# Optimization experiments

Hardware: AMD Instinct MI355X
Metric: run time of the kernel (lower is better)

Reference implementation:

```python
import jax, jax.numpy as jnp
import numpy as np

NHOP = 3

def setup_inputs() -> dict:
    key = jax.random.key(0)
    kq, kk, kv, kw, kb = jax.random.split(key, 5)
    B, Lq, Lk, D = 16, 512, 2048, 1024
    Q = jax.random.normal(kq, (B, Lq, D), dtype=jnp.float32)
    K = jax.random.normal(kk, (B, Lk, D), dtype=jnp.float32)
    V = jax.random.normal(kv, (B, Lk, D), dtype=jnp.float32)
    # nn.Linear(2D, D): weight [D, 2D], bias [D]
    W = jax.random.normal(kw, (D, 2 * D), dtype=jnp.float32) * (1.0 / np.sqrt(2 * D))
    b = jax.random.normal(kb, (D,), dtype=jnp.float32) * 0.01
    return {"Q": Q, "K": K, "V": V, "W": W, "b": b}


def reference(Q, K, V, W, b):
    D = Q.shape[-1]
    scale = 1.0 / jnp.sqrt(jnp.asarray(D, dtype=Q.dtype))
    Q_hop = Q
    attn = None
    for _ in range(NHOP):
        # [B, Lq, Lk]
        scores = jnp.einsum("bqd,bkd->bqk", Q_hop, K) * scale
        attn = jax.nn.softmax(scores, axis=-1)
        R = jnp.einsum("bqk,bkd->bqd", attn, V)          # [B, Lq, D]
        cat = jnp.concatenate([Q_hop, R], axis=-1)       # [B, Lq, 2D]
        Q_hop = jnp.tanh(jnp.einsum("bqe,de->bqd", cat, W) + b)
    return (Q_hop, attn)
```

## Files before the change

kernel.cpp:

```cpp
#include <hip/hip_runtime.h>
#include <math.h>

#define NB 16
#define LQ 512
#define LKK 2048
#define DD 1024

typedef _Float16 half8 __attribute__((ext_vector_type(8)));
typedef _Float16 half4 __attribute__((ext_vector_type(4)));
typedef float f32x4 __attribute__((ext_vector_type(4)));

__device__ __forceinline__ void gl_lds16(const void* g, void* l) {
    __builtin_amdgcn_global_load_lds(
        (const __attribute__((address_space(1))) void*)g,
        (__attribute__((address_space(3))) void*)l, 16, 0, 0);
}

__global__ __launch_bounds__(512, 2) void gemm_qk_256(
    const _Float16* __restrict__ A, long sA,
    const _Float16* __restrict__ B, long sB,
    _Float16* __restrict__ P, long sP,
    float* __restrict__ partial,
    float scale)
{
    __shared__ _Float16 lsA[2][256 * 64];
    __shared__ _Float16 lsB[2][256 * 64];
    const int tid = threadIdx.x;
    const int w = tid >> 6, l = tid & 63;
    const int wr = w >> 2, wc = w & 3;
    const int lrg = l >> 4, lc = l & 15, lr = lrg << 2;

    int id = blockIdx.x + gridDim.x * (blockIdx.y + gridDim.y * blockIdx.z);
    const int nwg = gridDim.x * gridDim.y * gridDim.z;
    id = (id & 7) * (nwg >> 3) + (id >> 3);
    const int bx = id % gridDim.x;
    const int t2 = id / gridDim.x;
    const int by = t2 % gridDim.y;
    const int z  = t2 / gridDim.y;
    const int m0 = by * 256, n0 = bx * 256;

    const _Float16* Ab = A + (size_t)z * sA + (size_t)m0 * DD;
    const _Float16* Bb = B + (size_t)z * sB + (size_t)n0 * DD;

    const int srow = l >> 3;
    const int sk = ((l & 7) ^ srow) << 3;

#define STG(dst, srcbase)                                                     \
    do {                                                                      \
        _Pragma("unroll")                                                     \
        for (int rr = 0; rr < 2; ++rr) {                                      \
            const int c = w + 8 * rr;                                         \
            gl_lds16((srcbase) + (size_t)(c * 8 + srow) * DD + sk,            \
                     (dst) + c * 512);                                        \
        }                                                                     \
    } while (0)

    half8 af[4][2], bf01[2][2], bf23[2][2];
    f32x4 acc[8][4] = {};
    const int rsb = (lc & 7) << 4;

#define LDA(buf, mh)                                                          \
    do {                                                                      \
        const char* p_ = (const char*)lsA[buf];                               \
        _Pragma("unroll")                                                     \
        for (int ii = 0; ii < 4; ++ii) {                                      \
            const int row_ = wr * 128 + (mh) * 64 + ii * 16 + lc;             \
            _Pragma("unroll")                                                 \
            for (int kk = 0; kk < 2; ++kk)                                    \
                af[ii][kk] = *(const half8*)(p_ + row_ * 128 +                \
                             ((kk * 64 + (lrg << 4)) ^ rsb));                 \
        }                                                                     \
    } while (0)

#define LDB(buf, nh, bfr)                                                     \
    do {                                                                      \
        const char* p_ = (const char*)lsB[buf];                               \
        _Pragma("unroll")                                                     \
        for (int jj = 0; jj < 2; ++jj) {                                      \
            const int row_ = wc * 64 + ((nh) * 2 + jj) * 16 + lc;             \
            _Pragma("unroll")                                                 \
            for (int kk = 0; kk < 2; ++kk)                                    \
                bfr[jj][kk] = *(const half8*)(p_ + row_ * 128 +               \
                              ((kk * 64 + (lrg << 4)) ^ rsb));                \
        }                                                                     \
    } while (0)

#define MM(mh, nh, bfr)                                                       \
    do {                                                                      \
        __builtin_amdgcn_s_setprio(1);                                        \
        _Pragma("unroll")                                                     \
        for (int ii = 0; ii < 4; ++ii)                                        \
            _Pragma("unroll")                                                 \
            for (int jj = 0; jj < 2; ++jj)                                    \
                _Pragma("unroll")                                             \
                for (int kk = 0; kk < 2; ++kk)                                \
                    acc[(mh) * 4 + ii][(nh) * 2 + jj] =                       \
                        __builtin_amdgcn_mfma_f32_16x16x32_f16(               \
                            af[ii][kk], bfr[jj][kk],                          \
                            acc[(mh) * 4 + ii][(nh) * 2 + jj], 0, 0, 0);      \
        __builtin_amdgcn_s_setprio(0);                                        \
    } while (0)

#define BAR __builtin_amdgcn_s_barrier()
#define VMW(n) asm volatile("s_waitcnt vmcnt(" #n ")" ::: "memory")

    STG(&lsA[0][0], Ab);
    STG(&lsA[0][128 * 64], Ab + (size_t)128 * DD);
    STG(&lsB[0][0], Bb);
    STG(&lsB[0][128 * 64], Bb + (size_t)128 * DD);
    STG(&lsA[1][0], Ab + 64);
    VMW(2);
    BAR;

    for (int i = 0; i < 7; ++i) {
        const int kt1 = (2 * i + 1) * 64, kt2 = kt1 + 64, kt3 = kt2 + 64;
        LDA(0, 0); LDB(0, 0, bf01);
        STG(&lsA[1][128 * 64], Ab + (size_t)128 * DD + kt1);
        BAR; MM(0, 0, bf01); BAR;
        LDB(0, 1, bf23);
        STG(&lsB[1][0], Bb + kt1);
        BAR; MM(0, 1, bf23); BAR;
        LDA(0, 1);
        STG(&lsB[1][128 * 64], Bb + (size_t)128 * DD + kt1);
        BAR; MM(1, 0, bf01); BAR;
        STG(&lsA[0][0], Ab + kt2);
        BAR; MM(1, 1, bf23);
        VMW(2); BAR;
        LDA(1, 0); LDB(1, 0, bf01);
        STG(&lsA[0][128 * 64], Ab + (size_t)128 * DD + kt2);
        BAR; MM(0, 0, bf01); BAR;
        LDB(1, 1, bf23);
        STG(&lsB[0][0], Bb + kt2);
        BAR; MM(0, 1, bf23); BAR;
        LDA(1, 1);
        STG(&lsB[0][128 * 64], Bb + (size_t)128 * DD + kt2);
        BAR; MM(1, 0, bf01); BAR;
        STG(&lsA[1][0], Ab + kt3);
        BAR; MM(1, 1, bf23);
        VMW(2); BAR;
    }
    {
        const int kt1 = 15 * 64;
        LDA(0, 0); LDB(0, 0, bf01);
        STG(&lsA[1][128 * 64], Ab + (size_t)128 * DD + kt1);
        BAR; MM(0, 0, bf01); BAR;
        LDB(0, 1, bf23);
        STG(&lsB[1][0], Bb + kt1);
        BAR; MM(0, 1, bf23); BAR;
        LDA(0, 1);
        STG(&lsB[1][128 * 64], Bb + (size_t)128 * DD + kt1);
        BAR; MM(1, 0, bf01); BAR;
        BAR; MM(1, 1, bf23);
        VMW(0); BAR;
        LDA(1, 0); LDB(1, 0, bf01);
        BAR; MM(0, 0, bf01); BAR;
        LDB(1, 1, bf23);
        BAR; MM(0, 1, bf23); BAR;
        LDA(1, 1);
        BAR; MM(1, 0, bf01); BAR;
        BAR; MM(1, 1, bf23);
    }
    __syncthreads();

    _Float16* Cb = P + (size_t)z * sP;
    float* psum = (float*)&lsA[0][0];
    #pragma unroll
    for (int i = 0; i < 8; ++i) {
        float rsum[4] = {0.f, 0.f, 0.f, 0.f};
        #pragma unroll
        for (int j = 0; j < 4; ++j) {
            const int n = n0 + wc * 64 + j * 16 + lc;
            #pragma unroll
            for (int r = 0; r < 4; ++r) {
                const int m = m0 + wr * 128 + i * 16 + lr + r;
                const float e = __expf(acc[i][j][r] * scale);
                Cb[(size_t)m * LKK + n] = (_Float16)e;
                rsum[r] += e;
            }
        }
        #pragma unroll
        for (int r = 0; r < 4; ++r) {
            float s = rsum[r];
            s += __shfl_xor(s, 1);
            s += __shfl_xor(s, 2);
            s += __shfl_xor(s, 4);
            s += __shfl_xor(s, 8);
            if (lc == 0) psum[(wr * 128 + i * 16 + lr + r) * 4 + wc] = s;
        }
    }
    __syncthreads();
    if (tid < 256) {
        const float* pr = psum + tid * 4;
        partial[((size_t)z * LQ + m0 + tid) * 8 + bx] = pr[0] + pr[1] + pr[2] + pr[3];
    }
#undef STG
#undef LDA
#undef LDB
#undef MM
}

__global__ __launch_bounds__(512, 2) void gemm_pc_256x128(
    const _Float16* __restrict__ Alo, long sAlo, int lda_lo,
    const _Float16* __restrict__ Ahi, long sAhi, int lda_hi,
    int ksplit,
    const _Float16* __restrict__ B, long sB, int ldb,
    int K, int mode,
    float* __restrict__ out32, long s32, int ldc32,
    _Float16* __restrict__ out16, long s16, int ldc16,
    const float* __restrict__ bias,
    const float* __restrict__ partial, int npart)
{
    __shared__ _Float16 ls[3][384 * 64];
    const int tid = threadIdx.x;
    const int w = tid >> 6, l = tid & 63;
    const int wr = w >> 2, wc = w & 3;
    const int lrg = l >> 4, lc = l & 15, lr = lrg << 2;

    int id = blockIdx.x + gridDim.x * (blockIdx.y + gridDim.y * blockIdx.z);
    const int nwg = gridDim.x * gridDim.y * gridDim.z;
    id = (id & 7) * (nwg >> 3) + (id >> 3);
    const int bx = id % gridDim.x;
    const int t2_ = id / gridDim.x;
    const int by = t2_ % gridDim.y;
    const int z  = t2_ / gridDim.y;
    const int m0 = by * 256, n0 = bx * 128;

    const _Float16* Abase_lo = Alo + (size_t)z * sAlo + (size_t)m0 * lda_lo;
    const _Float16* Abase_hi = Ahi ? (Ahi + (size_t)z * sAhi + (size_t)m0 * lda_hi) : (const _Float16*)0;
    const _Float16* Bbase = B + (size_t)z * sB + (size_t)n0 * ldb;

    const int srow = l >> 3;
    const int sk = ((l & 7) ^ srow) << 3;
    const int rsb = (lc & 7) << 4;

    half8 af[4][2], bf[2][2];
    f32x4 acc[8][2] = {};

#define STGA(tt, dbuf)                                                        \
    do {                                                                      \
        const int kb_ = (tt) * 64;                                            \
        const _Float16* s_; int ld_;                                          \
        if (kb_ < ksplit) { s_ = Abase_lo + kb_;           ld_ = lda_lo; }    \
        else              { s_ = Abase_hi + (kb_ - ksplit); ld_ = lda_hi; }   \
        _Float16* d_ = &ls[dbuf][0];                                          \
        _Pragma("unroll")                                                     \
        for (int rr = 0; rr < 4; ++rr) {                                      \
            const int c = w + 8 * rr;                                         \
            gl_lds16(s_ + (size_t)(c * 8 + srow) * ld_ + sk, d_ + c * 512);   \
        }                                                                     \
    } while (0)

#define STGB(tt, dbuf)                                                        \
    do {                                                                      \
        const _Float16* s_ = Bbase + (tt) * 64;                               \
        _Float16* d_ = &ls[dbuf][256 * 64];                                   \
        _Pragma("unroll")                                                     \
        for (int rr = 0; rr < 2; ++rr) {                                      \
            const int c = w + 8 * rr;                                         \
            gl_lds16(s_ + (size_t)(c * 8 + srow) * ldb + sk, d_ + c * 512);   \
        }                                                                     \
    } while (0)

#define LDA2(buf, mh)                                                         \
    do {                                                                      \
        const char* p_ = (const char*)&ls[buf][0];                            \
        _Pragma("unroll")                                                     \
        for (int ii = 0; ii < 4; ++ii) {                                      \
            const int row_ = wr * 128 + (mh) * 64 + ii * 16 + lc;             \
            _Pragma("unroll")                                                 \
            for (int kk = 0; kk < 2; ++kk)                                    \
                af[ii][kk] = *(const half8*)(p_ + row_ * 128 +                \
                             ((kk * 64 + (lrg << 4)) ^ rsb));                 \
        }                                                                     \
    } while (0)

#define LDB2(buf)                                                             \
    do {                                                                      \
        const char* p_ = (const char*)&ls[buf][256 * 64];                     \
        _Pragma("unroll")                                                     \
        for (int jj = 0; jj < 2; ++jj) {                                      \
            const int row_ = wc * 32 + jj * 16 + lc;                          \
            _Pragma("unroll")                                                 \
            for (int kk = 0; kk < 2; ++kk)                                    \
                bf[jj][kk] = *(const half8*)(p_ + row_ * 128 +                \
                              ((kk * 64 + (lrg << 4)) ^ rsb));                \
        }                                                                     \
    } while (0)

#define MM2(mh)                                                               \
    do {                                                                      \
        __builtin_amdgcn_s_setprio(1);                                        \
        _Pragma("unroll")                                                     \
        for (int ii = 0; ii < 4; ++ii)                                        \
            _Pragma("unroll")                                                 \
            for (int jj = 0; jj < 2; ++jj)                                    \
                _Pragma("unroll")                                             \
                for (int kk = 0; kk < 2; ++kk)                                \
                    acc[(mh) * 4 + ii][jj] =                                  \
                        __builtin_amdgcn_mfma_f32_16x16x32_f16(               \
                            af[ii][kk], bf[jj][kk],                           \
                            acc[(mh) * 4 + ii][jj], 0, 0, 0);                 \
        __builtin_amdgcn_s_setprio(0);                                        \
    } while (0)

    const int NT = K >> 6;
    STGA(0, 0); STGB(0, 0);
    STGA(1, 1); STGB(1, 1);
    VMW(6);
    BAR;

    int b = 0, b2 = 2;
    for (int t = 0; t < NT; ++t) {
        const int tt = t + 2;
        const bool st = tt < NT;
        LDA2(b, 0); LDB2(b);
        if (st) STGA(tt, b2);
        BAR; MM2(0); BAR;
        LDA2(b, 1);
        if (st) STGB(tt, b2);
        BAR; MM2(1);
        if (t < NT - 2)       VMW(6);
        else if (t == NT - 2) VMW(0);
        BAR;
        b = (b == 2) ? 0 : b + 1;
        b2 = (b2 == 2) ? 0 : b2 + 1;
    }
    __syncthreads();

    if (mode == 1) {
        float* psum = (float*)&ls[0][0];
        if (tid < 256) {
            const float* pp = partial + ((size_t)z * LQ + m0 + tid) * npart;
            float s = 0.0f;
            for (int c = 0; c < npart; ++c) s += pp[c];
            psum[tid] = 1.0f / s;
        }
        __syncthreads();
        _Float16* Cb = out16 + (size_t)z * s16;
        #pragma unroll
        for (int i = 0; i < 8; ++i)
            #pragma unroll
            for (int j = 0; j < 2; ++j) {
                const int n = n0 + wc * 32 + j * 16 + lc;
                #pragma unroll
                for (int r = 0; r < 4; ++r) {
                    const int ml = wr * 128 + i * 16 + lr + r;
                    Cb[(size_t)(m0 + ml) * ldc16 + n] =
                        (_Float16)(acc[i][j][r] * psum[ml]);
                }
            }
    } else {
        float bv[2];
        #pragma unroll
        for (int j = 0; j < 2; ++j)
            bv[j] = bias[n0 + wc * 32 + j * 16 + lc];
        #pragma unroll
        for (int i = 0; i < 8; ++i)
            #pragma unroll
            for (int j = 0; j < 2; ++j) {
                const int n = n0 + wc * 32 + j * 16 + lc;
                #pragma unroll
                for (int r = 0; r < 4; ++r) {
                    const int m = m0 + wr * 128 + i * 16 + lr + r;
                    const float t = tanhf(acc[i][j][r] + bv[j]);
                    if (out16) out16[(size_t)z * s16 + (size_t)m * ldc16 + n] = (_Float16)t;
                    if (out32) out32[(size_t)z * s32 + (size_t)m * ldc32 + n] = t;
                }
            }
    }
#undef STGA
#undef STGB
#undef LDA2
#undef LDB2
#undef MM2
#undef BAR
#undef VMW
}

__global__ __launch_bounds__(256) void gemm_f16_nt(
    const _Float16* __restrict__ Alo, long sAlo, int lda_lo,
    const _Float16* __restrict__ Ahi, long sAhi, int lda_hi,
    int ksplit,
    const _Float16* __restrict__ B, long sB, int ldb,
    int K, int mode, float scale,
    float* __restrict__ out32, long s32, int ldc32,
    _Float16* __restrict__ out16, long s16, int ldc16,
    const float* __restrict__ bias,
    float* __restrict__ partial, const float* __restrict__ inv, int npart)
{
    __shared__ _Float16 lsA[128 * 64];
    __shared__ _Float16 lsB[128 * 64];
    __shared__ float psum[128][2];
    const int tid = threadIdx.x;
    const int w = tid >> 6, l = tid & 63;
    const int wr = w >> 1, wc = w & 1;

    int id = blockIdx.x + gridDim.x * (blockIdx.y + gridDim.y * blockIdx.z);
    const int nwg = gridDim.x * gridDim.y * gridDim.z;
    id = (id & 7) * (nwg >> 3) + (id >> 3);
    const int bx = id % gridDim.x;
    const int t2 = id / gridDim.x;
    const int by = t2 % gridDim.y;
    const int z = t2 / gridDim.y;
    const int m0 = by * 128, n0 = bx * 128;

    const _Float16* Abase_lo = Alo + (size_t)z * sAlo + (size_t)m0 * lda_lo;
    const _Float16* Abase_hi = Ahi ? (Ahi + (size_t)z * sAhi + (size_t)m0 * lda_hi) : (const _Float16*)0;
    const _Float16* Bbase = B + (size_t)z * sB + (size_t)n0 * ldb;

    const int srow = l >> 3;
    const int sswz = ((l & 7) ^ srow) << 3;

    f32x4 acc[4][4] = {};

    for (int k0 = 0; k0 < K; k0 += 64) {
        const _Float16* Ap; int kloc, ldaA;
        if (k0 < ksplit) { Ap = Abase_lo; kloc = k0;          ldaA = lda_lo; }
        else             { Ap = Abase_hi; kloc = k0 - ksplit; ldaA = lda_hi; }
        #pragma unroll
        for (int i = 0; i < 4; ++i) {
            const int c = w * 4 + i;
            const int row = c * 8 + srow;
            gl_lds16(Ap + (size_t)row * ldaA + kloc + sswz, &lsA[c * 512]);
        }
        #pragma unroll
        for (int i = 0; i < 4; ++i) {
            const int c = w * 4 + i;
            const int row = c * 8 + srow;
            gl_lds16(Bbase + (size_t)row * ldb + k0 + sswz, &lsB[c * 512]);
        }
        __syncthreads();

        half8 af[4][2], bf[4][2];
        const char* lA = (const char*)lsA;
        const char* lB = (const char*)lsB;
        const int rs = (l & 7) << 4;
        const int cb = (l >> 4) << 4;
        #pragma unroll
        for (int i = 0; i < 4; ++i) {
            const int rowa = wr * 64 + i * 16 + (l & 15);
            const int rowb = wc * 64 + i * 16 + (l & 15);
            #pragma unroll
            for (int kk = 0; kk < 2; ++kk) {
                af[i][kk] = *(const half8*)(lA + rowa * 128 + ((kk * 64 + cb) ^ rs));
                bf[i][kk] = *(const half8*)(lB + rowb * 128 + ((kk * 64 + cb) ^ rs));
            }
        }
        #pragma unroll
        for (int kk = 0; kk < 2; ++kk)
            #pragma unroll
            for (int i = 0; i < 4; ++i)
                #pragma unroll
                for (int j = 0; j < 4; ++j)
                    acc[i][j] = __builtin_amdgcn_mfma_f32_16x16x32_f16(
                        af[i][kk], bf[j][kk], acc[i][j], 0, 0, 0);
        __syncthreads();
    }

    const int lr = (l >> 4) * 4;
    const int lc = l & 15;
    if (mode == 0) {
        _Float16* Cb = out16 + (size_t)z * s16;
        float rsum[4][4];
        #pragma unroll
        for (int i = 0; i < 4; ++i)
            #pragma unroll
            for (int r = 0; r < 4; ++r) rsum[i][r] = 0.0f;
        #pragma unroll
        for (int i = 0; i < 4; ++i)
            #pragma unroll
            for (int j = 0; j < 4; ++j) {
                const int n = n0 + wc * 64 + j * 16 + lc;
                #pragma unroll
                for (int r = 0; r < 4; ++r) {
                    const int m = m0 + wr * 64 + i * 16 + lr + r;
                    const float e = __expf(acc[i][j][r] * scale);
                    Cb[(size_t)m * ldc16 + n] = (_Float16)e;
                    rsum[i][r] += e;
                }
            }
        #pragma unroll
        for (int i = 0; i < 4; ++i)
            #pragma unroll
            for (int r = 0; r < 4; ++r) {
                float s = rsum[i][r];
                s += __shfl_xor(s, 1);
                s += __shfl_xor(s, 2);
                s += __shfl_xor(s, 4);
                s += __shfl_xor(s, 8);
                rsum[i][r] = s;
            }
        if (lc == 0) {
            #pragma unroll
            for (int i = 0; i < 4; ++i)
                #pragma unroll
                for (int r = 0; r < 4; ++r)
                    psum[wr * 64 + i * 16 + lr + r][wc] = rsum[i][r];
        }
        __syncthreads();
        if (tid < 128)
            partial[((size_t)z * LQ + m0 + tid) * npart + bx] = psum[tid][0] + psum[tid][1];
    } else if (mode == 1) {
        _Float16* Cb = out16 + (size_t)z * s16;
        float iv[4][4];
        if (partial) {
            if (tid < 128) {
                const float* pp = partial + ((size_t)z * LQ + m0 + tid) * npart;
                float s = 0.0f;
                for (int c = 0; c < npart; ++c) s += pp[c];
                psum[tid][0] = 1.0f / s;
            }
            __syncthreads();
            #pragma unroll
            for (int i = 0; i < 4; ++i)
                #pragma unroll
                for (int r = 0; r < 4; ++r)
                    iv[i][r] = psum[wr * 64 + i * 16 + lr + r][0];
        } else {
            #pragma unroll
            for (int i = 0; i < 4; ++i)
                #pragma unroll
                for (int r = 0; r < 4; ++r)
                    iv[i][r] = inv ? inv[(size_t)z * LQ + m0 + wr * 64 + i * 16 + lr + r] : 1.0f;
        }
        #pragma unroll
        for (int i = 0; i < 4; ++i)
            #pragma unroll
            for (int j = 0; j < 4; ++j) {
                const int n = n0 + wc * 64 + j * 16 + lc;
                #pragma unroll
                for (int r = 0; r < 4; ++r) {
                    const int m = m0 + wr * 64 + i * 16 + lr + r;
                    Cb[(size_t)m * ldc16 + n] = (_Float16)(acc[i][j][r] * iv[i][r]);
                }
            }
    } else if (mode == 4) {
        float* Cb = out32 + (size_t)z * s32;
        #pragma unroll
        for (int i = 0; i < 4; ++i)
            #pragma unroll
            for (int j = 0; j < 4; ++j) {
                const int n = n0 + wc * 64 + j * 16 + lc;
                #pragma unroll
                for (int r = 0; r < 4; ++r) {
                    const int m = m0 + wr * 64 + i * 16 + lr + r;
                    Cb[(size_t)m * ldc32 + n] = acc[i][j][r] * scale;
                }
            }
    } else {
        float bv[4];
        #pragma unroll
        for (int j = 0; j < 4; ++j)
            bv[j] = bias[n0 + wc * 64 + j * 16 + lc];
        #pragma unroll
        for (int i = 0; i < 4; ++i)
            #pragma unroll
            for (int j = 0; j < 4; ++j) {
                const int n = n0 + wc * 64 + j * 16 + lc;
                #pragma unroll
                for (int r = 0; r < 4; ++r) {
                    const int m = m0 + wr * 64 + i * 16 + lr + r;
                    const float t = tanhf(acc[i][j][r] + bv[j]);
                    if (out16) out16[(size_t)z * s16 + (size_t)m * ldc16 + n] = (_Float16)t;
                    if (out32) out32[(size_t)z * s32 + (size_t)m * ldc32 + n] = t;
                }
            }
    }
}

__global__ __launch_bounds__(256) void scale_attn(
    const _Float16* __restrict__ P, const float* __restrict__ partial,
    float* __restrict__ attn, int npart)
{
    __shared__ float sinv;
    const long row = blockIdx.x;
    const int tid = threadIdx.x;
    if (tid < npart) {
        float s = partial[row * npart + tid];
        for (int off = npart >> 1; off > 0; off >>= 1) s += __shfl_xor(s, off);
        if (tid == 0) sinv = 1.0f / s;
    }
    __syncthreads();
    const float inv = sinv;
    const half8 h = *(const half8*)(P + row * 2048 + tid * 8);
    float* o = attn + row * 2048 + tid * 8;
    float4 a = make_float4((float)h[0] * inv, (float)h[1] * inv,
                           (float)h[2] * inv, (float)h[3] * inv);
    float4 b = make_float4((float)h[4] * inv, (float)h[5] * inv,
                           (float)h[6] * inv, (float)h[7] * inv);
    *(float4*)o = a;
    *(float4*)(o + 4) = b;
}

__global__ __launch_bounds__(256) void make_inv(
    const float* __restrict__ partial, float* __restrict__ inv)
{
    const int row = blockIdx.x * 256 + threadIdx.x;
    const float4 a = *(const float4*)(partial + (size_t)row * 16);
    const float4 b = *(const float4*)(partial + (size_t)row * 16 + 4);
    const float4 c = *(const float4*)(partial + (size_t)row * 16 + 8);
    const float4 d = *(const float4*)(partial + (size_t)row * 16 + 12);
    const float s = (a.x + a.y + a.z + a.w) + (b.x + b.y + b.z + b.w)
                  + (c.x + c.y + c.z + c.w) + (d.x + d.y + d.z + d.w);
    inv[row] = 1.0f / s;
}

__global__ __launch_bounds__(256) void softmax_rows2(
    float* __restrict__ S, _Float16* __restrict__ f16out,
    long f16stride, int write_f32)
{
    __shared__ float red[8];
    const long row = blockIdx.x;
    float* p = S + row * LKK;
    const int tid = threadIdx.x;
    float4 v0 = ((const float4*)p)[tid];
    float4 v1 = ((const float4*)p)[tid + 256];
    float m = fmaxf(fmaxf(fmaxf(v0.x, v0.y), fmaxf(v0.z, v0.w)),
                    fmaxf(fmaxf(v1.x, v1.y), fmaxf(v1.z, v1.w)));
    #pragma unroll
    for (int off = 32; off > 0; off >>= 1) m = fmaxf(m, __shfl_down(m, off));
    if ((tid & 63) == 0) red[tid >> 6] = m;
    __syncthreads();
    m = fmaxf(fmaxf(red[0], red[1]), fmaxf(red[2], red[3]));
    v0.x = expf(v0.x - m); v0.y = expf(v0.y - m);
    v0.z = expf(v0.z - m); v0.w = expf(v0.w - m);
    v1.x = expf(v1.x - m); v1.y = expf(v1.y - m);
    v1.z = expf(v1.z - m); v1.w = expf(v1.w - m);
    float s = v0.x + v0.y + v0.z + v0.w + v1.x + v1.y + v1.z + v1.w;
    #pragma unroll
    for (int off = 32; off > 0; off >>= 1) s += __shfl_down(s, off);
    if ((tid & 63) == 0) red[4 + (tid >> 6)] = s;
    __syncthreads();
    s = red[4] + red[5] + red[6] + red[7];
    const float inv = 1.0f / s;
    v0.x *= inv; v0.y *= inv; v0.z *= inv; v0.w *= inv;
    v1.x *= inv; v1.y *= inv; v1.z *= inv; v1.w *= inv;
    if (write_f32) {
        ((float4*)p)[tid] = v0;
        ((float4*)p)[tid + 256] = v1;
    }
    _Float16* q = f16out + row * f16stride;
    half4 h0 = { (_Float16)v0.x, (_Float16)v0.y, (_Float16)v0.z, (_Float16)v0.w };
    half4 h1 = { (_Float16)v1.x, (_Float16)v1.y, (_Float16)v1.z, (_Float16)v1.w };
    *(half4*)(q + tid * 4) = h0;
    *(half4*)(q + 1024 + tid * 4) = h1;
}

__global__ __launch_bounds__(256) void cvt_f32_to_f16(
    const float* __restrict__ in, _Float16* __restrict__ out, long n)
{
    const long i = ((long)blockIdx.x * 256 + threadIdx.x) * 8;
    if (i + 8 > n) return;
    float4 a = *(const float4*)(in + i);
    float4 b = *(const float4*)(in + i + 4);
    half8 h = { (_Float16)a.x, (_Float16)a.y, (_Float16)a.z, (_Float16)a.w,
                (_Float16)b.x, (_Float16)b.y, (_Float16)b.z, (_Float16)b.w };
    *(half8*)(out + i) = h;
}

__global__ __launch_bounds__(256) void transpose_cvt_v(
    const float* __restrict__ V, _Float16* __restrict__ Vt)
{
    __shared__ _Float16 t[64][80];
    const int z = blockIdx.z;
    const int k0 = blockIdx.y * 64, d0 = blockIdx.x * 64;
    const float* Vb = V + (size_t)z * LKK * DD;
    _Float16* Vtb = Vt + (size_t)z * DD * LKK;
    const int r = threadIdx.x >> 2;
    const int c0 = (threadIdx.x & 3) * 16;
    #pragma unroll
    for (int j = 0; j < 4; ++j) {
        float4 v = *(const float4*)(Vb + (size_t)(k0 + r) * DD + d0 + c0 + j * 4);
        t[c0 + j * 4 + 0][r] = (_Float16)v.x;
        t[c0 + j * 4 + 1][r] = (_Float16)v.y;
        t[c0 + j * 4 + 2][r] = (_Float16)v.z;
        t[c0 + j * 4 + 3][r] = (_Float16)v.w;
    }
    __syncthreads();
    #pragma unroll
    for (int j = 0; j < 2; ++j) {
        half8 h = *(const half8*)&t[r][c0 + j * 8];
        *(half8*)(Vtb + (size_t)(d0 + r) * LKK + k0 + c0 + j * 8) = h;
    }
}

constexpr int TM = 64, TN = 64, TK = 32;
constexpr int PAD = 4;

__global__ __launch_bounds__(256) void gemm_nt_k(
    const float* __restrict__ A, int lda, long sA,
    const float* __restrict__ Bt, int ldb, long sB,
    float* __restrict__ C, int ldc, long sC, int K, float scale)
{
    __shared__ float As[TK][TM + PAD];
    __shared__ float Bs[TK][TN + PAD];
    const float* Ab = A + (long)blockIdx.z * sA;
    const float* Bb = Bt + (long)blockIdx.z * sB;
    float* Cb = C + (long)blockIdx.z * sC;
    const int m0 = blockIdx.y * TM, n0 = blockIdx.x * TN;
    const int tid = threadIdx.x;
    const int tn = tid & 15, tm = tid >> 4;
    float acc[4][4] = {};
    for (int k0 = 0; k0 < K; k0 += TK) {
        #pragma unroll
        for (int c = tid; c < (TM * TK) / 4; c += 256) {
            const int row = c >> 3, kc = (c & 7) << 2;
            const float4 g = *(const float4*)(Ab + (long)(m0 + row) * lda + (k0 + kc));
            As[kc + 0][row] = g.x; As[kc + 1][row] = g.y;
            As[kc + 2][row] = g.z; As[kc + 3][row] = g.w;
        }
        #pragma unroll
        for (int c = tid; c < (TN * TK) / 4; c += 256) {
            const int row = c >> 3, kc = (c & 7) << 2;
            const float4 g = *(const float4*)(Bb + (long)(n0 + row) * ldb + (k0 + kc));
            Bs[kc + 0][row] = g.x; Bs[kc + 1][row] = g.y;
            Bs[kc + 2][row] = g.z; Bs[kc + 3][row] = g.w;
        }
        __syncthreads();
        #pragma unroll
        for (int kk = 0; kk < TK; ++kk) {
            const float4 av = *(const float4*)&As[kk][tm << 2];
            const float4 bv = *(const float4*)&Bs[kk][tn << 2];
            const float a[4] = {av.x, av.y, av.z, av.w};
            const float b[4] = {bv.x, bv.y, bv.z, bv.w};
            #pragma unroll
            for (int i = 0; i < 4; ++i)
                #pragma unroll
                for (int j = 0; j < 4; ++j)
                    acc[i][j] = fmaf(a[i], b[j], acc[i][j]);
        }
        __syncthreads();
    }
    #pragma unroll
    for (int i = 0; i < 4; ++i) {
        float4 o = make_float4(acc[i][0] * scale, acc[i][1] * scale,
                               acc[i][2] * scale, acc[i][3] * scale);
        *(float4*)(Cb + (long)(m0 + (tm << 2) + i) * ldc + n0 + (tn << 2)) = o;
    }
}

__global__ __launch_bounds__(256) void gemm_nn_k(
    const float* __restrict__ A, int lda, long sA,
    const float* __restrict__ B, int ldb, long sB,
    float* __restrict__ C, int ldc, long sC, int K)
{
    __shared__ float As[TK][TM + PAD];
    __shared__ float Bs[TK][TN + PAD];
    const float* Ab = A + (long)blockIdx.z * sA;
    const float* Bb = B + (long)blockIdx.z * sB;
    float* Cb = C + (long)blockIdx.z * sC;
    const int m0 = blockIdx.y * TM, n0 = blockIdx.x * TN;
    const int tid = threadIdx.x;
    const int tn = tid & 15, tm = tid >> 4;
    float acc[4][4] = {};
    for (int k0 = 0; k0 < K; k0 += TK) {
        #pragma unroll
        for (int c = tid; c < (TM * TK) / 4; c += 256) {
            const int row = c >> 3, kc = (c & 7) << 2;
            const float4 g = *(const float4*)(Ab + (long)(m0 + row) * lda + (k0 + kc));
            As[kc + 0][row] = g.x; As[kc + 1][row] = g.y;
            As[kc + 2][row] = g.z; As[kc + 3][row] = g.w;
        }
        #pragma unroll
        for (int c = tid; c < (TK * TN) / 4; c += 256) {
            const int krow = c >> 4, nc = (c & 15) << 2;
            *(float4*)&Bs[krow][nc] =
                *(const float4*)(Bb + (long)(k0 + krow) * ldb + n0 + nc);
        }
        __syncthreads();
        #pragma unroll
        for (int kk = 0; kk < TK; ++kk) {
            const float4 av = *(const float4*)&As[kk][tm << 2];
            const float4 bv = *(const float4*)&Bs[kk][tn << 2];
            const float a[4] = {av.x, av.y, av.z, av.w};
            const float b[4] = {bv.x, bv.y, bv.z, bv.w};
            #pragma unroll
            for (int i = 0; i < 4; ++i)
                #pragma unroll
                for (int j = 0; j < 4; ++j)
                    acc[i][j] = fmaf(a[i], b[j], acc[i][j]);
        }
        __syncthreads();
    }
    #pragma unroll
    for (int i = 0; i < 4; ++i) {
        float4 o = make_float4(acc[i][0], acc[i][1], acc[i][2], acc[i][3]);
        *(float4*)(Cb + (long)(m0 + (tm << 2) + i) * ldc + n0 + (tn << 2)) = o;
    }
}

__global__ __launch_bounds__(256) void gemm_cat_k(
    const float* __restrict__ Qh, const float* __restrict__ R,
    const float* __restrict__ W, const float* __restrict__ bias,
    float* __restrict__ C)
{
    __shared__ float As[TK][TM + PAD];
    __shared__ float Bs[TK][TN + PAD];
    const float* Qb = Qh + (long)blockIdx.z * LQ * DD;
    const float* Rb = R + (long)blockIdx.z * LQ * DD;
    float* Cb = C + (long)blockIdx.z * LQ * DD;
    const int m0 = blockIdx.y * TM, n0 = blockIdx.x * TN;
    const int tid = threadIdx.x;
    const int tn = tid & 15, tm = tid >> 4;
    float acc[4][4] = {};
    for (int k0 = 0; k0 < 2 * DD; k0 += TK) {
        const float* src = (k0 < DD) ? Qb : Rb;
        const int kb = (k0 < DD) ? k0 : k0 - DD;
        #pragma unroll
        for (int c = tid; c < (TM * TK) / 4; c += 256) {
            const int row = c >> 3, kc = (c & 7) << 2;
            const float4 g = *(const float4*)(src + (long)(m0 + row) * DD + (kb + kc));
            As[kc + 0][row] = g.x; As[kc + 1][row] = g.y;
            As[kc + 2][row] = g.z; As[kc + 3][row] = g.w;
        }
        #pragma unroll
        for (int c = tid; c < (TN * TK) / 4; c += 256) {
            const int row = c >> 3, kc = (c & 7) << 2;
            const float4 g = *(const float4*)(W + (long)(n0 + row) * (2 * DD) + (k0 + kc));
            Bs[kc + 0][row] = g.x; Bs[kc + 1][row] = g.y;
            Bs[kc + 2][row] = g.z; Bs[kc + 3][row] = g.w;
        }
        __syncthreads();
        #pragma unroll
        for (int kk = 0; kk < TK; ++kk) {
            const float4 av = *(const float4*)&As[kk][tm << 2];
            const float4 bv = *(const float4*)&Bs[kk][tn << 2];
            const float a[4] = {av.x, av.y, av.z, av.w};
            const float b[4] = {bv.x, bv.y, bv.z, bv.w};
            #pragma unroll
            for (int i = 0; i < 4; ++i)
                #pragma unroll
                for (int j = 0; j < 4; ++j)
                    acc[i][j] = fmaf(a[i], b[j], acc[i][j]);
        }
        __syncthreads();
    }
    #pragma unroll
    for (int i = 0; i < 4; ++i) {
        float4 o;
        o.x = tanhf(acc[i][0] + bias[n0 + (tn << 2) + 0]);
        o.y = tanhf(acc[i][1] + bias[n0 + (tn << 2) + 1]);
        o.z = tanhf(acc[i][2] + bias[n0 + (tn << 2) + 2]);
        o.w = tanhf(acc[i][3] + bias[n0 + (tn << 2) + 3]);
        *(float4*)(Cb + (long)(m0 + (tm << 2) + i) * DD + n0 + (tn << 2)) = o;
    }
}

__global__ __launch_bounds__(256) void softmax_rows(float* __restrict__ S) {
    __shared__ float red[8];
    float* p = S + (size_t)blockIdx.x * LKK;
    const int tid = threadIdx.x;
    float4 v0 = ((const float4*)p)[tid];
    float4 v1 = ((const float4*)p)[tid + 256];
    float m = fmaxf(fmaxf(fmaxf(v0.x, v0.y), fmaxf(v0.z, v0.w)),
                    fmaxf(fmaxf(v1.x, v1.y), fmaxf(v1.z, v1.w)));
    #pragma unroll
    for (int off = 32; off > 0; off >>= 1) m = fmaxf(m, __shfl_down(m, off));
    if ((tid & 63) == 0) red[tid >> 6] = m;
    __syncthreads();
    m = fmaxf(fmaxf(red[0], red[1]), fmaxf(red[2], red[3]));
    v0.x = expf(v0.x - m); v0.y = expf(v0.y - m);
    v0.z = expf(v0.z - m); v0.w = expf(v0.w - m);
    v1.x = expf(v1.x - m); v1.y = expf(v1.y - m);
    v1.z = expf(v1.z - m); v1.w = expf(v1.w - m);
    float s = v0.x + v0.y + v0.z + v0.w + v1.x + v1.y + v1.z + v1.w;
    #pragma unroll
    for (int off = 32; off > 0; off >>= 1) s += __shfl_down(s, off);
    if ((tid & 63) == 0) red[4 + (tid >> 6)] = s;
    __syncthreads();
    s = red[4] + red[5] + red[6] + red[7];
    const float inv = 1.0f / s;
    v0.x *= inv; v0.y *= inv; v0.z *= inv; v0.w *= inv;
    v1.x *= inv; v1.y *= inv; v1.z *= inv; v1.w *= inv;
    ((float4*)p)[tid] = v0;
    ((float4*)p)[tid + 256] = v1;
}

extern "C" void kernel_launch(void* const* d_in, const int* in_sizes, int n_in,
                              void* d_out, int out_size, void* d_ws, size_t ws_size,
                              hipStream_t stream) {
    const float* Q    = (const float*)d_in[0];
    const float* Km   = (const float*)d_in[1];
    const float* V    = (const float*)d_in[2];
    const float* W    = (const float*)d_in[3];
    const float* bias = (const float*)d_in[4];
    const float scale = 0.03125f;
    dim3 blk(256);

    const size_t NEED_FULL = 189267968ULL;
    const size_t NEED_R3   = 155189248ULL;

    if (ws_size >= NEED_FULL) {
        char* ws = (char*)d_ws;
        _Float16* Kh     = (_Float16*)ws;
        _Float16* Vt     = (_Float16*)(ws + 67108864);
        _Float16* Wh     = (_Float16*)(ws + 134217728);
        _Float16* Rh     = (_Float16*)(ws + 138412032);
        _Float16* Qping  = (_Float16*)(ws + 155189248);
        _Float16* Qpong  = (_Float16*)(ws + 171966464);
        float*    partialB = (float*)(ws + 188743680);

        float*    outQ  = (float*)d_out;
        _Float16* P2    = (_Float16*)d_out;
        float*    attnF = (float*)((char*)d_out + 33554432);
        _Float16* P01   = (_Float16*)attnF;

        cvt_f32_to_f16<<<4096, blk, 0, stream>>>(Q, Qping, (long)NB * LQ * DD);
        cvt_f32_to_f16<<<16384, blk, 0, stream>>>(Km, Kh, (long)NB * LKK * DD);
        cvt_f32_to_f16<<<1024, blk, 0, stream>>>(W, Wh, (long)DD * 2 * DD);
        transpose_cvt_v<<<dim3(DD / 64, LKK / 64, NB), blk, 0, stream>>>(V, Vt);

        dim3 gS2(LKK / 256, LQ / 256, NB);
        dim3 gP(DD / 128, LQ / 256, NB);

        for (int h = 0; h < 3; ++h) {
            _Float16* qcur = (h == 1) ? Qpong : Qping;
            _Float16* P    = (h == 2) ? P2 : P01;

            gemm_qk_256<<<gS2, dim3(512), 0, stream>>>(
                qcur, (long)LQ * DD, Kh, (long)LKK * DD,
                P, (long)LQ * LKK, partialB, scale);
            if (h == 2)
                scale_attn<<<NB * LQ, blk, 0, stream>>>(P2, partialB, attnF, 8);
            gemm_pc_256x128<<<gP, dim3(512), 0, stream>>>(
                P, (long)LQ * LKK, LKK,
                (const _Float16*)0, 0, 0, LKK * 16,
                Vt, (long)DD * LKK, LKK,
                LKK, 1,
                (float*)0, 0, 0,
                Rh, (long)LQ * DD, DD,
                (const float*)0, partialB, 8);
            _Float16* qn = (h == 0) ? Qpong : (h == 1) ? Qping : (_Float16*)0;
            float* fo = (h == 2) ? outQ : (float*)0;
            gemm_pc_256x128<<<gP, dim3(512), 0, stream>>>(
                qcur, (long)LQ * DD, DD,
                Rh, (long)LQ * DD, DD, DD,
                Wh, 0, 2 * DD,
                2 * DD, 2,
                fo, (long)LQ * DD, DD,
                qn, (long)LQ * DD, DD,
                bias, (const float*)0, 0);
        }
    } else if (ws_size >= NEED_R3) {
        char* ws = (char*)d_ws;
        _Float16* Kh  = (_Float16*)ws;
        _Float16* Vt  = (_Float16*)(ws + 67108864);
        _Float16* Wh  = (_Float16*)(ws + 134217728);
        _Float16* Rh  = (_Float16*)(ws + 138412032);
        _Float16* attn2 = (_Float16*)ws;
        float* Fout = (float*)(ws + 33554432);

        _Float16* Qping = (_Float16*)d_out;
        _Float16* Qpong = Qping + (size_t)NB * LQ * DD;
        float* S = (float*)((char*)d_out + 33554432);
        _Float16* P = (_Float16*)S;
        float* partialB = (float*)((char*)d_out + 73400320);
        float* invB     = (float*)((char*)d_out + 73924608);

        cvt_f32_to_f16<<<4096, blk, 0, stream>>>(Q, Qping, (long)NB * LQ * DD);
        cvt_f32_to_f16<<<16384, blk, 0, stream>>>(Km, Kh, (long)NB * LKK * DD);
        cvt_f32_to_f16<<<1024, blk, 0, stream>>>(W, Wh, (long)DD * 2 * DD);
        transpose_cvt_v<<<dim3(DD / 64, LKK / 64, NB), blk, 0, stream>>>(V, Vt);

        dim3 gS(LKK / 128, LQ / 128, NB);
        dim3 gR(DD / 128, LQ / 128, NB);

        for (int h = 0; h < 3; ++h) {
            _Float16* qcur = (h == 1) ? Qpong : Qping;
            if (h < 2) {
                gemm_f16_nt<<<gS, blk, 0, stream>>>(
                    qcur, (long)LQ * DD, DD, (const _Float16*)0, 0, 0, DD,
                    Kh, (long)LKK * DD, DD, DD,
                    0, scale, (float*)0, 0, 0,
                    P, (long)LQ * LKK, LKK, (const float*)0,
                    partialB, (const float*)0, 16);
                make_inv<<<32, blk, 0, stream>>>(partialB, invB);
                gemm_f16_nt<<<gR, blk, 0, stream>>>(
                    P, (long)LQ * LKK, LKK,
                    (const _Float16*)0, 0, 0, LKK,
                    Vt, (long)DD * LKK, LKK, LKK,
                    1, 1.0f, (float*)0, 0, 0,
                    Rh, (long)LQ * DD, DD, (const float*)0,
                    (float*)0, invB, 0);
            } else {
                gemm_f16_nt<<<gS, blk, 0, stream>>>(
                    qcur, (long)LQ * DD, DD, (const _Float16*)0, 0, 0, DD,
                    Kh, (long)LKK * DD, DD, DD,
                    4, scale, S, (long)LQ * LKK, LKK,
                    (_Float16*)0, 0, 0, (const float*)0,
                    (float*)0, (const float*)0, 0);
                softmax_rows2<<<NB * LQ, blk, 0, stream>>>(S, attn2, 2048L, 1);
                gemm_f16_nt<<<gR, blk, 0, stream>>>(
                    attn2, (long)LQ * LKK, LKK,
                    (const _Float16*)0, 0, 0, LKK,
                    Vt, (long)DD * LKK, LKK, LKK,
                    1, 1.0f, (float*)0, 0, 0,
                    Rh, (long)LQ * DD, DD, (const float*)0,
                    (float*)0, (const float*)0, 0);
            }
            _Float16* qn = (h == 0) ? Qpong : (h == 1) ? Qping : (_Float16*)0;
            float* fo = (h == 2) ? Fout : (float*)0;
            gemm_f16_nt<<<gR, blk, 0, stream>>>(
                qcur, (long)LQ * DD, DD,
                Rh, (long)LQ * DD, DD, DD,
                Wh, 0, 2 * DD, 2 * DD,
                2, 1.0f, fo, (long)LQ * DD, DD,
                qn, (long)LQ * DD, DD, bias,
                (float*)0, (const float*)0, 0);
        }
        hipMemcpyAsync(d_out, Fout, 33554432ULL, hipMemcpyDeviceToDevice, stream);
    } else {
        float* outQ = (float*)d_out;
        float* S    = outQ + (size_t)NB * LQ * DD;
        float* R    = (float*)d_ws;
        float* T    = R + (size_t)NB * LQ * DD;
        dim3 gS(LKK / TN, LQ / TM, NB);
        dim3 gR(DD / TN, LQ / TM, NB);
        for (int h = 0; h < 3; ++h) {
            const float* Qh = (h == 0) ? Q : (h == 1 ? (const float*)T : (const float*)outQ);
            float* cout = (h == 1) ? outQ : T;
            gemm_nt_k<<<gS, blk, 0, stream>>>(Qh, DD, (long)LQ * DD, Km, DD, (long)LKK * DD,
                                              S, LKK, (long)LQ * LKK, DD, scale);
            softmax_rows<<<NB * LQ, blk, 0, stream>>>(S);
            gemm_nn_k<<<gR, blk, 0, stream>>>(S, LKK, (long)LQ * LKK, V, DD, (long)LKK * DD,
                                              R, DD, (long)LQ * DD, LKK);
            gemm_cat_k<<<gR, blk, 0, stream>>>(Qh, R, W, bias, cout);
        }
        hipMemcpyAsync(outQ, T, (size_t)NB * LQ * DD * sizeof(float),
                       hipMemcpyDeviceToDevice, stream);
    }
}
```

Before: 500.2 us.

## Reshape PV/proj GEMM wave tiling to 4x2 waves and fuse f16 conversions

The 256x128 GEMM now arranges its 8 waves as 4 row-groups by 2 column-groups, so each wave owns a 64x64 sub-tile instead of 128x32. The A fragment is loaded once per k-step and the B fragment is loaded in two halves, which changes the LDS read mix and aims for a more balanced fragment reuse. Separately, the three fp32-to-fp16 conversion launches for Q, K and W are merged into one grid-stride kernel to save launch overhead. The fixed 2048-block grid-stride loop may expose less memory parallelism than the original per-element launches.

```diff
diff --git a/kernel.cpp b/kernel.cpp
--- a/kernel.cpp
+++ b/kernel.cpp
@@ -213,7 +213,7 @@
     __shared__ _Float16 ls[3][384 * 64];
     const int tid = threadIdx.x;
     const int w = tid >> 6, l = tid & 63;
-    const int wr = w >> 2, wc = w & 3;
+    const int wr = w >> 1, wc = w & 1;
     const int lrg = l >> 4, lc = l & 15, lr = lrg << 2;
 
     int id = blockIdx.x + gridDim.x * (blockIdx.y + gridDim.y * blockIdx.z);
@@ -234,7 +234,7 @@
     const int rsb = (lc & 7) << 4;
 
     half8 af[4][2], bf[2][2];
-    f32x4 acc[8][2] = {};
+    f32x4 acc[4][4] = {};
 
 #define STGA(tt, dbuf)                                                        \
     do {                                                                      \
@@ -261,12 +261,12 @@
         }                                                                     \
     } while (0)
 
-#define LDA2(buf, mh)                                                         \
+#define LDA2(buf)                                                             \
     do {                                                                      \
         const char* p_ = (const char*)&ls[buf][0];                            \
         _Pragma("unroll")                                                     \
         for (int ii = 0; ii < 4; ++ii) {                                      \
-            const int row_ = wr * 128 + (mh) * 64 + ii * 16 + lc;             \
+            const int row_ = wr * 64 + ii * 16 + lc;                          \
             _Pragma("unroll")                                                 \
             for (int kk = 0; kk < 2; ++kk)                                    \
                 af[ii][kk] = *(const half8*)(p_ + row_ * 128 +                \
@@ -274,12 +274,12 @@
         }                                                                     \
     } while (0)
 
-#define LDB2(buf)                                                             \
+#define LDB2(buf, nh)                                                         \
     do {                                                                      \
         const char* p_ = (const char*)&ls[buf][256 * 64];                     \
         _Pragma("unroll")                                                     \
         for (int jj = 0; jj < 2; ++jj) {                                      \
-            const int row_ = wc * 32 + jj * 16 + lc;                          \
+            const int row_ = wc * 64 + ((nh) * 2 + jj) * 16 + lc;             \
             _Pragma("unroll")                                                 \
             for (int kk = 0; kk < 2; ++kk)                                    \
                 bf[jj][kk] = *(const half8*)(p_ + row_ * 128 +                \
@@ -287,7 +287,7 @@
         }                                                                     \
     } while (0)
 
-#define MM2(mh)                                                               \
+#define MM2(nh)                                                               \
     do {                                                                      \
         __builtin_amdgcn_s_setprio(1);                                        \
         _Pragma("unroll")                                                     \
@@ -296,10 +296,10 @@
             for (int jj = 0; jj < 2; ++jj)                                    \
                 _Pragma("unroll")                                             \
                 for (int kk = 0; kk < 2; ++kk)                                \
-                    acc[(mh) * 4 + ii][jj] =                                  \
+                    acc[ii][(nh) * 2 + jj] =                                  \
                         __builtin_amdgcn_mfma_f32_16x16x32_f16(               \
                             af[ii][kk], bf[jj][kk],                           \
-                            acc[(mh) * 4 + ii][jj], 0, 0, 0);                 \
+                            acc[ii][(nh) * 2 + jj], 0, 0, 0);                 \
         __builtin_amdgcn_s_setprio(0);                                        \
     } while (0)
 
@@ -313,10 +313,10 @@
     for (int t = 0; t < NT; ++t) {
         const int tt = t + 2;
         const bool st = tt < NT;
-        LDA2(b, 0); LDB2(b);
+        LDA2(b); LDB2(b, 0);
         if (st) STGA(tt, b2);
         BAR; MM2(0); BAR;
-        LDA2(b, 1);
+        LDB2(b, 1);
         if (st) STGB(tt, b2);
         BAR; MM2(1);
         if (t < NT - 2)       VMW(6);
@@ -338,30 +338,30 @@
         __syncthreads();
         _Float16* Cb = out16 + (size_t)z * s16;
         #pragma unroll
-        for (int i = 0; i < 8; ++i)
-            #pragma unroll
-            for (int j = 0; j < 2; ++j) {
-                const int n = n0 + wc * 32 + j * 16 + lc;
+        for (int i = 0; i < 4; ++i)
+            #pragma unroll
+            for (int j = 0; j < 4; ++j) {
+                const int n = n0 + wc * 64 + j * 16 + lc;
                 #pragma unroll
                 for (int r = 0; r < 4; ++r) {
-                    const int ml = wr * 128 + i * 16 + lr + r;
+                    const int ml = wr * 64 + i * 16 + lr + r;
                     Cb[(size_t)(m0 + ml) * ldc16 + n] =
                         (_Float16)(acc[i][j][r] * psum[ml]);
                 }
             }
     } else {
-        float bv[2];
-        #pragma unroll
-        for (int j = 0; j < 2; ++j)
-            bv[j] = bias[n0 + wc * 32 + j * 16 + lc];
-        #pragma unroll
-        for (int i = 0; i < 8; ++i)
-            #pragma unroll
-            for (int j = 0; j < 2; ++j) {
-                const int n = n0 + wc * 32 + j * 16 + lc;
+        float bv[4];
+        #pragma unroll
+        for (int j = 0; j < 4; ++j)
+            bv[j] = bias[n0 + wc * 64 + j * 16 + lc];
+        #pragma unroll
+        for (int i = 0; i < 4; ++i)
+            #pragma unroll
+            for (int j = 0; j < 4; ++j) {
+                const int n = n0 + wc * 64 + j * 16 + lc;
                 #pragma unroll
                 for (int r = 0; r < 4; ++r) {
-                    const int m = m0 + wr * 128 + i * 16 + lr + r;
+                    const int m = m0 + wr * 64 + i * 16 + lr + r;
                     const float t = tanhf(acc[i][j][r] + bv[j]);
                     if (out16) out16[(size_t)z * s16 + (size_t)m * ldc16 + n] = (_Float16)t;
                     if (out32) out32[(size_t)z * s32 + (size_t)m * ldc32 + n] = t;
@@ -646,6 +646,31 @@
     *(half4*)(q + 1024 + tid * 4) = h1;
 }
 
+__global__ __launch_bounds__(256) void cvt3(
+    const float* __restrict__ Q, const float* __restrict__ K,
+    const float* __restrict__ W,
+    _Float16* __restrict__ Qh, _Float16* __restrict__ Kh,
+    _Float16* __restrict__ Wh)
+{
+    const long nQ = (long)NB * LQ * DD;
+    const long nK = (long)NB * LKK * DD;
+    const long nW = (long)DD * 2 * DD;
+    const long total = (nQ + nK + nW) >> 3;
+    for (long c = (long)blockIdx.x * 256 + threadIdx.x; c < total;
+         c += (long)gridDim.x * 256) {
+        const long i = c << 3;
+        const float* src; _Float16* dst; long off;
+        if (i < nQ)           { src = Q; dst = Qh; off = i; }
+        else if (i < nQ + nK) { src = K; dst = Kh; off = i - nQ; }
+        else                  { src = W; dst = Wh; off = i - nQ - nK; }
+        float4 a = *(const float4*)(src + off);
+        float4 b = *(const float4*)(src + off + 4);
+        half8 h = { (_Float16)a.x, (_Float16)a.y, (_Float16)a.z, (_Float16)a.w,
+                    (_Float16)b.x, (_Float16)b.y, (_Float16)b.z, (_Float16)b.w };
+        *(half8*)(dst + off) = h;
+    }
+}
+
 __global__ __launch_bounds__(256) void cvt_f32_to_f16(
     const float* __restrict__ in, _Float16* __restrict__ out, long n)
 {
@@ -905,9 +930,7 @@
         float*    attnF = (float*)((char*)d_out + 33554432);
         _Float16* P01   = (_Float16*)attnF;
 
-        cvt_f32_to_f16<<<4096, blk, 0, stream>>>(Q, Qping, (long)NB * LQ * DD);
-        cvt_f32_to_f16<<<16384, blk, 0, stream>>>(Km, Kh, (long)NB * LKK * DD);
-        cvt_f32_to_f16<<<1024, blk, 0, stream>>>(W, Wh, (long)DD * 2 * DD);
+        cvt3<<<2048, blk, 0, stream>>>(Q, Km, W, Qping, Kh, Wh);
         transpose_cvt_v<<<dim3(DD / 64, LKK / 64, NB), blk, 0, stream>>>(V, Vt);
 
         dim3 gS2(LKK / 256, LQ / 256, NB);
```

New measurement: 494.6 us. Within noise of the previous version (-1.1%).
